# Optimization experiments

Measured on AMD Instinct MI355X. Metric: run time of the kernel, lower is better.

Reference implementation:

```python
import jax, jax.numpy as jnp
import numpy as np

N = 50000          # total nodes (2 types x 25000)
E = 400000         # edges
NEG = 0.2          # leaky_relu negative slope


def _seg_softmax(e, dst, n):
    # softmax over edges grouped by destination node
    m = jax.ops.segment_max(e, dst, num_segments=n)
    m = jnp.where(jnp.isfinite(m), m, 0.0)
    ex = jnp.exp(e - m[dst])
    s = jax.ops.segment_sum(ex, dst, num_segments=n)
    return ex / (s[dst] + 1e-16)


def _gat_conv(h, src, dst, W, al, ar, b, heads, out, res=None, act=None):
    n = h.shape[0]
    ft = (h @ W).reshape(n, heads, out)               # [N,H,D]
    el = jnp.sum(ft * al, axis=-1)                    # [N,H]
    er = jnp.sum(ft * ar, axis=-1)                    # [N,H]
    e = jax.nn.leaky_relu(el[src] + er[dst], NEG)     # [E,H]
    alpha = _seg_softmax(e, dst, n)                   # [E,H]
    rst = jax.ops.segment_sum(ft[src] * alpha[:, :, None], dst, num_segments=n)
    if isinstance(res, str):                          # identity residual (in == heads*out)
        rst = rst + h.reshape(n, heads, out)
    elif res is not None:                             # linear residual projection
        rst = rst + (h @ res).reshape(n, heads, out)
    rst = rst + b                                     # bias [H,D]
    if act is not None:
        rst = act(rst)
    return rst


def setup_inputs() -> dict:
    key = jax.random.key(0)
    ks = jax.random.split(key, 24)
    g = lambda i, shp, s=0.05: jax.random.normal(ks[i], shp, jnp.float32) * s
    inp = {
        "x0": jax.random.normal(ks[0], (25000, 256), jnp.float32),
        "x1": jax.random.normal(ks[1], (25000, 256), jnp.float32),
        "src": jax.random.randint(ks[2], (E,), 0, N, jnp.int32).astype(jnp.int64),
        "dst": jax.random.randint(ks[3], (E,), 0, N, jnp.int32).astype(jnp.int64),
        # per-type input projections
        "fc0_W": g(4, (256, 64)), "fc0_b": jnp.zeros((64,), jnp.float32),
        "fc1_W": g(5, (256, 64)), "fc1_b": jnp.zeros((64,), jnp.float32),
        # layer 0: 64 -> 8 heads x 64
        "W0": g(6, (64, 512)), "al0": g(7, (8, 64)), "ar0": g(8, (8, 64)), "b0": jnp.zeros((8, 64), jnp.float32),
        # layer 1: 512 -> 8 heads x 64 (identity residual)
        "W1": g(9, (512, 512)), "al1": g(10, (8, 64)), "ar1": g(11, (8, 64)), "b1": jnp.zeros((8, 64), jnp.float32),
        # output layer: 512 -> 1 head x 16 (linear residual)
        "W2": g(12, (512, 16)), "al2": g(13, (1, 16)), "ar2": g(14, (1, 16)), "b2": jnp.zeros((1, 16), jnp.float32),
        "resW2": g(15, (512, 16)),
    }
    return inp


def reference(x0, x1, src, dst, fc0_W, fc0_b, fc1_W, fc1_b,
              W0, al0, ar0, b0, W1, al1, ar1, b1,
              W2, al2, ar2, b2, resW2):
    # per-type linear projections, then concat over node axis
    h = jnp.concatenate([x0 @ fc0_W + fc0_b, x1 @ fc1_W + fc1_b], axis=0)  # [N,64]
    h = _gat_conv(h, src, dst, W0, al0, ar0, b0, 8, 64, None, jax.nn.elu).reshape(N, -1)
    h = _gat_conv(h, src, dst, W1, al1, ar1, b1, 8, 64, "id", jax.nn.elu).reshape(N, -1)
    encoded = h
    logits = _gat_conv(h, src, dst, W2, al2, ar2, b2, 1, 16, resW2, None).mean(axis=1)  # [N,16]
    return (logits, encoded)
```

## Files before the change

kernel.cpp:

```cpp
#include <hip/hip_runtime.h>
#include <hip/hip_bf16.h>
#include <math.h>

typedef __hip_bfloat16 bf16;
typedef __attribute__((ext_vector_type(8))) short short8;
typedef __attribute__((ext_vector_type(8))) unsigned short ushort8;
typedef __attribute__((ext_vector_type(4))) float floatx4;

#define NNODES 50000
#define NHALF  25000
#define NEDGES 400000
#define NEG_SLOPE 0.2f

__device__ __forceinline__ float b2f(bf16 x){ return __bfloat162float(x); }
__device__ __forceinline__ bf16  f2b(float x){ return __float2bfloat16(x); }
__device__ __forceinline__ float u2f(unsigned short u){ return __uint_as_float(((unsigned)u) << 16); }

__device__ __forceinline__ float loadF(const void* p, long i, int f32){
  return f32 ? ((const float*)p)[i] : b2f(((const bf16*)p)[i]);
}
__device__ __forceinline__ void storeOut(void* p, long i, float v, int f32){
  if (f32) ((float*)p)[i] = v; else ((bf16*)p)[i] = f2b(v);
}

__device__ __forceinline__ void gl_lds16(const bf16* g, short* l){
  __builtin_amdgcn_global_load_lds(
      (const __attribute__((address_space(1))) unsigned int*)g,
      (__attribute__((address_space(3))) unsigned int*)l, 16, 0, 0);
}

__global__ void k_detect(const unsigned short* __restrict__ x0u,
                         const unsigned* __restrict__ dstu,
                         int* __restrict__ flags)
{
  __shared__ int sh_insane;
  __shared__ unsigned sh_or;
  if (threadIdx.x == 0) { sh_insane = 0; sh_or = 0u; }
  __syncthreads();
  int insane = 0; unsigned orv = 0u;
  for (int i = threadIdx.x; i < 2048; i += 256) {
    unsigned short w = x0u[2 * i];
    int ex = (w >> 7) & 0xFF;
    if (w != 0 && (ex < 108 || ex > 142)) insane++;
    orv |= dstu[2 * i + 1];
  }
  atomicAdd(&sh_insane, insane);
  atomicOr(&sh_or, orv);
  __syncthreads();
  if (threadIdx.x == 0) {
    flags[0] = (sh_insane > 512) ? 1 : 0;
    flags[1] = (sh_or == 0u) ? 1 : 0;
  }
}

__global__ void k_conv_idx(const int* __restrict__ sraw, const int* __restrict__ draw,
                           int* __restrict__ s32, int* __restrict__ d32,
                           int* __restrict__ deg,
                           const int* __restrict__ flags)
{
  int e = blockIdx.x * blockDim.x + threadIdx.x;
  if (e >= NEDGES) return;
  int stride = flags[1] ? 2 : 1;
  int s = sraw[(long)e * stride];
  int d = draw[(long)e * stride];
  s32[e] = s;
  d32[e] = d;
  atomicAdd(&deg[d], 1);
}

struct WSrc { const void* p[17]; int n[17]; };

__global__ void k_canon(WSrc w, bf16* __restrict__ out, const int* __restrict__ flags,
                        int total)
{
  int f32 = flags[0];
  for (int t = blockIdx.x * blockDim.x + threadIdx.x; t < total;
       t += gridDim.x * blockDim.x) {
    int idx = t, k = 0;
    while (idx >= w.n[k]) { idx -= w.n[k]; k++; }
    out[t] = f2b(loadF(w.p[k], idx, f32));
  }
}

__global__ void k_convx(const void* __restrict__ x0, const void* __restrict__ x1,
                        bf16* __restrict__ xb, const int* __restrict__ flags)
{
  long t = (long)blockIdx.x * blockDim.x + threadIdx.x;
  if (t >= (long)NNODES * 256) return;
  int f32 = flags[0];
  long half = (long)NHALF * 256;
  float v = (t < half) ? loadF(x0, t, f32) : loadF(x1, t - half, f32);
  xb[t] = f2b(v);
}

__global__ void k_wt(const bf16* __restrict__ W, bf16* __restrict__ Wt,
                     int K, int M, int Mpad)
{
  int t = blockIdx.x * blockDim.x + threadIdx.x;
  if (t >= Mpad * K) return;
  int m = t / K, k = t % K;
  Wt[t] = (m < M) ? W[(long)k * M + m] : f2b(0.f);
}

__global__ __launch_bounds__(256) void k_gemm_mfma(
    const bf16* __restrict__ A, const bf16* __restrict__ Wt,
    bf16* __restrict__ C, int N, int K, int ldc, int Mout,
    const bf16* __restrict__ bias)
{
  __shared__ __align__(16) short lsA[128 * 32];
  __shared__ __align__(16) short lsB[128 * 32];
  int tid = threadIdx.x;
  int wave = tid >> 6, lane = tid & 63;
  int wm = wave >> 1, wn = wave & 1;
  int rowBase = blockIdx.x * 128;
  int colBase = blockIdx.y * 128;

  floatx4 acc[4][4] = {};
  int laneRow = lane >> 2;
  int laneCol = (lane & 3) * 8;
  int cA0 = wave * 2, cA1 = cA0 + 1;

  for (int kb = 0; kb < K; kb += 32) {
    int r0 = rowBase + cA0 * 16 + laneRow; if (r0 > N - 1) r0 = N - 1;
    int r1 = rowBase + cA1 * 16 + laneRow; if (r1 > N - 1) r1 = N - 1;
    gl_lds16(A + (size_t)r0 * K + kb + laneCol, &lsA[cA0 * 512]);
    gl_lds16(A + (size_t)r1 * K + kb + laneCol, &lsA[cA1 * 512]);
    int m0 = colBase + cA0 * 16 + laneRow;
    int m1 = colBase + cA1 * 16 + laneRow;
    gl_lds16(Wt + (size_t)m0 * K + kb + laneCol, &lsB[cA0 * 512]);
    gl_lds16(Wt + (size_t)m1 * K + kb + laneCol, &lsB[cA1 * 512]);
    __syncthreads();

    short8 af[4], bfr[4];
    int lr = lane & 15, q8 = (lane >> 4) * 8;
    #pragma unroll
    for (int mt = 0; mt < 4; ++mt)
      af[mt] = *(const short8*)&lsA[(wm * 64 + mt * 16 + lr) * 32 + q8];
    #pragma unroll
    for (int nt = 0; nt < 4; ++nt)
      bfr[nt] = *(const short8*)&lsB[(wn * 64 + nt * 16 + lr) * 32 + q8];
    #pragma unroll
    for (int mt = 0; mt < 4; ++mt)
      #pragma unroll
      for (int nt = 0; nt < 4; ++nt)
        acc[mt][nt] = __builtin_amdgcn_mfma_f32_16x16x32_bf16(
            af[mt], bfr[nt], acc[mt][nt], 0, 0, 0);
    __syncthreads();
  }

  int lc = lane & 15, rq = (lane >> 4) * 4;
  #pragma unroll
  for (int mt = 0; mt < 4; ++mt) {
    #pragma unroll
    for (int nt = 0; nt < 4; ++nt) {
      int col = colBase + wn * 64 + nt * 16 + lc;
      if (col >= Mout) continue;
      float bsv = bias ? b2f(bias[col]) : 0.f;
      #pragma unroll
      for (int r = 0; r < 4; ++r) {
        int row = rowBase + wm * 64 + mt * 16 + rq + r;
        if (row < N) C[(size_t)row * ldc + col] = f2b(acc[mt][nt][r] + bsv);
      }
    }
  }
}

__global__ __launch_bounds__(256) void k_elr8(
    const bf16* __restrict__ ft,
    const bf16* __restrict__ al, const bf16* __restrict__ ar,
    float* __restrict__ el, float* __restrict__ er,
    float* __restrict__ part)
{
  __shared__ float sal[512], sar[512];
  __shared__ float redA[32], redB[32];
  for (int i = threadIdx.x; i < 512; i += 256) { sal[i] = b2f(al[i]); sar[i] = b2f(ar[i]); }
  __syncthreads();
  int tid = threadIdx.x;
  int t = blockIdx.x * 256 + tid;
  float a = -1e30f, b = -1e30f;
  if (t < NNODES * 8) {
    int n = t >> 3, h = t & 7;
    const unsigned short* f = (const unsigned short*)ft + (size_t)n * 512 + h * 64;
    float aa = 0.f, bb = 0.f;
    #pragma unroll
    for (int j = 0; j < 8; ++j) {
      ushort8 v = *(const ushort8*)&f[j * 8];
      #pragma unroll
      for (int k = 0; k < 8; ++k) {
        float x = u2f(v[k]);
        aa += x * sal[h * 64 + j * 8 + k];
        bb += x * sar[h * 64 + j * 8 + k];
      }
    }
    a = aa; b = bb;
    el[t] = a; er[t] = b;
  }
  #pragma unroll
  for (int off = 8; off <= 32; off <<= 1) {
    a = fmaxf(a, __shfl_xor(a, off));
    b = fmaxf(b, __shfl_xor(b, off));
  }
  int wave = tid >> 6, lane = tid & 63;
  if (lane < 8) { redA[wave * 8 + lane] = a; redB[wave * 8 + lane] = b; }
  __syncthreads();
  if (tid < 8) {
    float ma = -1e30f, mb = -1e30f;
    #pragma unroll
    for (int w2 = 0; w2 < 4; ++w2) {
      ma = fmaxf(ma, redA[w2 * 8 + tid]);
      mb = fmaxf(mb, redB[w2 * 8 + tid]);
    }
    part[blockIdx.x * 16 + tid]     = ma;
    part[blockIdx.x * 16 + 8 + tid] = mb;
  }
}

__global__ __launch_bounds__(256) void k_elr1(
    const bf16* __restrict__ ft2,
    const bf16* __restrict__ al, const bf16* __restrict__ ar,
    float* __restrict__ el, float* __restrict__ er,
    float* __restrict__ part)
{
  __shared__ float rA[4], rB[4];
  int tid = threadIdx.x;
  int n = blockIdx.x * 256 + tid;
  float a = -1e30f, b = -1e30f;
  if (n < NNODES) {
    const unsigned short* f = (const unsigned short*)ft2 + (size_t)n * 32;
    float aa = 0.f, bb = 0.f;
    #pragma unroll
    for (int d = 0; d < 16; ++d) {
      float x = u2f(f[d]);
      aa += x * b2f(al[d]);
      bb += x * b2f(ar[d]);
    }
    a = aa; b = bb;
    el[n] = a; er[n] = b;
  }
  #pragma unroll
  for (int off = 1; off <= 32; off <<= 1) {
    a = fmaxf(a, __shfl_xor(a, off));
    b = fmaxf(b, __shfl_xor(b, off));
  }
  int wave = tid >> 6, lane = tid & 63;
  if (lane == 0) { rA[wave] = a; rB[wave] = b; }
  __syncthreads();
  if (tid == 0) {
    float ma = -1e30f, mb = -1e30f;
    #pragma unroll
    for (int w2 = 0; w2 < 4; ++w2) { ma = fmaxf(ma, rA[w2]); mb = fmaxf(mb, rB[w2]); }
    part[blockIdx.x * 2]     = ma;
    part[blockIdx.x * 2 + 1] = mb;
  }
}

__global__ void k_maxfin(const float* __restrict__ part, float* __restrict__ M,
                         int nblk, int H)
{
  __shared__ float sm[256];
  __shared__ float sm2[16];
  int tid = threadIdx.x;
  int TH = 2 * H;
  int s = tid % TH, c = tid / TH;
  int nch = 256 / TH;
  float m = -1e30f;
  for (int b = c; b < nblk; b += nch) m = fmaxf(m, part[b * TH + s]);
  sm[tid] = m;
  __syncthreads();
  if (tid < TH) {
    float mm = -1e30f;
    for (int c2 = 0; c2 < nch; ++c2) mm = fmaxf(mm, sm[c2 * TH + tid]);
    sm2[tid] = mm;
  }
  __syncthreads();
  if (tid < H) {
    float v = sm2[tid] + sm2[H + tid];
    M[tid] = v > 0.f ? v : NEG_SLOPE * v;
  }
}

__global__ __launch_bounds__(1024) void k_bsum(const int* __restrict__ deg,
                                               int* __restrict__ bsum, int n)
{
  __shared__ int ws[16];
  int tid = threadIdx.x, lane = tid & 63, wv = tid >> 6;
  int i = blockIdx.x * 1024 + tid;
  int v = (i < n) ? deg[i] : 0;
  #pragma unroll
  for (int off = 1; off < 64; off <<= 1) v += __shfl_xor(v, off);
  if (lane == 0) ws[wv] = v;
  __syncthreads();
  if (tid < 16) {
    int s = ws[tid];
    #pragma unroll
    for (int off = 1; off < 16; off <<= 1) s += __shfl_xor(s, off);
    if (tid == 0) bsum[blockIdx.x] = s;
  }
}

__global__ void k_bscan(int* __restrict__ bsum, int* __restrict__ row_start,
                        int nb, int n)
{
  int lane = threadIdx.x;
  int v = (lane < nb) ? bsum[lane] : 0;
  int x = v;
  #pragma unroll
  for (int off = 1; off < 64; off <<= 1) {
    int y = __shfl_up(x, off);
    if (lane >= off) x += y;
  }
  if (lane < nb) bsum[lane] = x - v;
  if (lane == 63) row_start[n] = x;
}

__global__ __launch_bounds__(1024) void k_scan2(const int* __restrict__ deg,
                                                const int* __restrict__ boff,
                                                int* __restrict__ row_start, int n)
{
  __shared__ int ws[16];
  int tid = threadIdx.x, lane = tid & 63, wv = tid >> 6;
  int i = blockIdx.x * 1024 + tid;
  int v = (i < n) ? deg[i] : 0;
  int x = v;
  #pragma unroll
  for (int off = 1; off < 64; off <<= 1) {
    int y = __shfl_up(x, off);
    if (lane >= off) x += y;
  }
  if (lane == 63) ws[wv] = x;
  __syncthreads();
  if (wv == 0 && lane < 16) {
    int s = ws[lane];
    int xs = s;
    #pragma unroll
    for (int off = 1; off < 16; off <<= 1) {
      int y = __shfl_up(xs, off);
      if (lane >= off) xs += y;
    }
    ws[lane] = xs - s;
  }
  __syncthreads();
  if (i < n) row_start[i] = boff[blockIdx.x] + ws[wv] + x - v;
}

__global__ void k_fill(const int* __restrict__ src, const int* __restrict__ dst,
                       int* __restrict__ cursor, int* __restrict__ csr_src, int E)
{
  int e = blockIdx.x * blockDim.x + threadIdx.x;
  if (e < E) {
    int p = atomicAdd(&cursor[dst[e]], 1);
    csr_src[p] = src[e];
  }
}

__global__ __launch_bounds__(256) void k_agg8(
    const int* __restrict__ row_start, const int* __restrict__ csr_src,
    const float* __restrict__ el, const float* __restrict__ er,
    const float* __restrict__ M,
    const bf16* __restrict__ ft, const bf16* __restrict__ hin,
    const bf16* __restrict__ bias,
    bf16* __restrict__ hout, void* __restrict__ dout, long dout_off,
    const int* __restrict__ flags, int mode)
{
  int wv = (int)((blockIdx.x * blockDim.x + threadIdx.x) >> 6);
  int lane = threadIdx.x & 63;
  if (wv >= NNODES) return;
  int n = wv, g = lane >> 3;
  int st = row_start[n], en = row_start[n + 1];
  float Mh  = M[g];
  float ern = er[n * 8 + g];

  const unsigned short* ftS = (const unsigned short*)ft;
  float ssum = 0.f;
  float acc[8] = {};
  int i = st;
  for (; i + 4 <= en; i += 4) {
    int sn0 = csr_src[i],     sn1 = csr_src[i + 1];
    int sn2 = csr_src[i + 2], sn3 = csr_src[i + 3];
    float e0 = el[sn0 * 8 + g], e1 = el[sn1 * 8 + g];
    float e2 = el[sn2 * 8 + g], e3 = el[sn3 * 8 + g];
    ushort8 r0 = *(const ushort8*)&ftS[(size_t)sn0 * 512 + lane * 8];
    ushort8 r1 = *(const ushort8*)&ftS[(size_t)sn1 * 512 + lane * 8];
    ushort8 r2 = *(const ushort8*)&ftS[(size_t)sn2 * 512 + lane * 8];
    ushort8 r3 = *(const ushort8*)&ftS[(size_t)sn3 * 512 + lane * 8];
    float v0 = e0 + ern, v1 = e1 + ern, v2 = e2 + ern, v3 = e3 + ern;
    v0 = v0 > 0.f ? v0 : NEG_SLOPE * v0;
    v1 = v1 > 0.f ? v1 : NEG_SLOPE * v1;
    v2 = v2 > 0.f ? v2 : NEG_SLOPE * v2;
    v3 = v3 > 0.f ? v3 : NEG_SLOPE * v3;
    float w0 = __expf(v0 - Mh), w1 = __expf(v1 - Mh);
    float w2 = __expf(v2 - Mh), w3 = __expf(v3 - Mh);
    ssum += (w0 + w1) + (w2 + w3);
    #pragma unroll
    for (int j = 0; j < 8; ++j)
      acc[j] += (w0 * u2f(r0[j]) + w1 * u2f(r1[j]))
              + (w2 * u2f(r2[j]) + w3 * u2f(r3[j]));
  }
  for (; i < en; ++i) {
    int sn = csr_src[i];
    float v0 = el[sn * 8 + g] + ern;
    v0 = v0 > 0.f ? v0 : NEG_SLOPE * v0;
    float w0 = __expf(v0 - Mh);
    ushort8 r0 = *(const ushort8*)&ftS[(size_t)sn * 512 + lane * 8];
    ssum += w0;
    #pragma unroll
    for (int j = 0; j < 8; ++j)
      acc[j] += w0 * u2f(r0[j]);
  }

  float inv = ssum > 0.f ? 1.f / ssum : 0.f;
  int f32 = flags[0];
  short8 outv;
  float rr[8];
  #pragma unroll
  for (int j = 0; j < 8; ++j) {
    int col = lane * 8 + j;
    float r = acc[j] * inv + b2f(bias[col]);
    if (mode == 1) r += b2f(hin[(size_t)n * 512 + col]);
    r = r > 0.f ? r : expm1f(r);
    rr[j] = r;
    bf16 o = f2b(r);
    outv[j] = *(short*)&o;
  }
  *(short8*)&hout[(size_t)n * 512 + lane * 8] = outv;
  if (dout) {
    if (f32) {
      floatx4 o0, o1;
      #pragma unroll
      for (int j = 0; j < 4; ++j) { o0[j] = rr[j]; o1[j] = rr[j + 4]; }
      float* dp = (float*)dout + dout_off + (size_t)n * 512 + lane * 8;
      *(floatx4*)dp = o0;
      *(floatx4*)(dp + 4) = o1;
    } else {
      *(short8*)&((bf16*)dout)[dout_off + (size_t)n * 512 + lane * 8] = outv;
    }
  }
}

__global__ __launch_bounds__(256) void k_agg1(
    const int* __restrict__ row_start, const int* __restrict__ csr_src,
    const float* __restrict__ el, const float* __restrict__ er,
    const float* __restrict__ M,
    const bf16* __restrict__ ft2, const bf16* __restrict__ bias,
    void* __restrict__ dout, const int* __restrict__ flags)
{
  int wv = (int)((blockIdx.x * blockDim.x + threadIdx.x) >> 6);
  int lane = threadIdx.x & 63;
  if (wv >= NNODES) return;
  int n = wv, sub = lane >> 4, d = lane & 15;
  int st = row_start[n], en = row_start[n + 1];
  float M0 = M[0];
  float ern = er[n];
  float ssum = 0.f, acc = 0.f;
  for (int i = st + sub; i < en; i += 4) {
    int sn = csr_src[i];
    float v = el[sn] + ern;
    v = v > 0.f ? v : NEG_SLOPE * v;
    float ex = __expf(v - M0);
    acc  += ex * b2f(ft2[(size_t)sn * 32 + d]);
    ssum += ex;
  }
  acc  += __shfl_xor(acc, 16);  acc  += __shfl_xor(acc, 32);
  ssum += __shfl_xor(ssum, 16); ssum += __shfl_xor(ssum, 32);
  if (sub == 0) {
    float inv = ssum > 0.f ? 1.f / ssum : 0.f;
    float r = acc * inv + b2f(bias[d]) + b2f(ft2[(size_t)n * 32 + 16 + d]);
    storeOut(dout, (size_t)n * 16 + d, r, flags[0]);
  }
}

extern "C" void kernel_launch(void* const* d_in, const int* in_sizes, int n_in,
                              void* d_out, int out_size, void* d_ws, size_t ws_size,
                              hipStream_t stream)
{
  const void* x0   = d_in[0];
  const void* x1   = d_in[1];
  const int*  srcR = (const int*)d_in[2];
  const int*  dstR = (const int*)d_in[3];

  char* p = (char*)d_ws;
  auto alloc = [&](size_t bytes) { char* r = p; p += (bytes + 255) & ~(size_t)255; return r; };
  int*      flags     = (int*)  alloc(256);
  bf16*     wc        = (bf16*) alloc((size_t)347312 * 2);
  int*      src32     = (int*)  alloc((size_t)NEDGES * 4);
  int*      dst32     = (int*)  alloc((size_t)NEDGES * 4);
  bf16*     xb        = (bf16*) alloc((size_t)NNODES * 256 * 2);
  bf16*     h0        = (bf16*) alloc((size_t)NNODES * 64 * 2);
  bf16*     hB        = (bf16*) alloc((size_t)NNODES * 512 * 2);
  bf16*     ft        = (bf16*) alloc((size_t)NNODES * 512 * 2);
  bf16*     ft2       = (bf16*) alloc((size_t)NNODES * 32 * 2);
  float*    el        = (float*)alloc((size_t)NNODES * 8 * 4);
  float*    er        = (float*)alloc((size_t)NNODES * 8 * 4);
  int*      deg       = (int*)  alloc((size_t)NNODES * 4);
  int*      row_start = (int*)  alloc((size_t)(NNODES + 1) * 4);
  int*      cursor    = (int*)  alloc((size_t)NNODES * 4);
  int*      csr_src   = (int*)  alloc((size_t)NEDGES * 4);
  int*      bsum      = (int*)  alloc((size_t)64 * 4);
  float*    maxpart   = (float*)alloc((size_t)1600 * 16 * 4);
  float*    Mbuf      = (float*)alloc(256);
  bf16*     fc0t      = (bf16*) alloc((size_t)128 * 256 * 2);
  bf16*     fc1t      = (bf16*) alloc((size_t)128 * 256 * 2);
  bf16*     W0t       = (bf16*) alloc((size_t)512 * 64 * 2);
  bf16*     W1t       = (bf16*) alloc((size_t)512 * 512 * 2);
  bf16*     W2c       = (bf16*) alloc((size_t)128 * 512 * 2);

  const int B = 256;
  auto blk = [](long total, int b) { return (unsigned)((total + b - 1) / b); };
  const int NSCB = (NNODES + 1023) / 1024;

  k_detect<<<1, 256, 0, stream>>>((const unsigned short*)x0, (const unsigned*)dstR, flags);
  hipMemsetAsync(deg, 0, (size_t)NNODES * 4, stream);
  k_conv_idx<<<blk(NEDGES, B), B, 0, stream>>>(srcR, dstR, src32, dst32, deg, flags);

  WSrc wsrc;
  const int widx[17] = {4,5,6,7, 8,9,10,11, 12,13,14,15, 16,17,18,19, 20};
  const int wn[17]   = {16384,64,16384,64, 32768,512,512,512, 262144,512,512,512,
                        8192,16,16,16, 8192};
  int wtotal = 0;
  for (int i = 0; i < 17; ++i) { wsrc.p[i] = d_in[widx[i]]; wsrc.n[i] = wn[i]; wtotal += wn[i]; }
  k_canon<<<blk(wtotal, B), B, 0, stream>>>(wsrc, wc, flags, wtotal);
  k_convx<<<blk((long)NNODES * 256, B), B, 0, stream>>>(x0, x1, xb, flags);

  long woff[18]; woff[0] = 0;
  for (int i = 0; i < 17; ++i) woff[i + 1] = woff[i] + wn[i];
  const bf16 *fc0W = wc + woff[0],  *fc0b = wc + woff[1];
  const bf16 *fc1W = wc + woff[2],  *fc1b = wc + woff[3];
  const bf16 *W0   = wc + woff[4],  *al0  = wc + woff[5],  *ar0 = wc + woff[6],  *b0 = wc + woff[7];
  const bf16 *W1   = wc + woff[8],  *al1  = wc + woff[9],  *ar1 = wc + woff[10], *b1 = wc + woff[11];
  const bf16 *W2   = wc + woff[12], *al2  = wc + woff[13], *ar2 = wc + woff[14], *b2 = wc + woff[15];
  const bf16 *resW2= wc + woff[16];

  k_wt<<<blk(128 * 256, B), B, 0, stream>>>(fc0W, fc0t, 256, 64, 128);
  k_wt<<<blk(128 * 256, B), B, 0, stream>>>(fc1W, fc1t, 256, 64, 128);
  k_wt<<<blk(512 * 64, B), B, 0, stream>>>(W0, W0t, 64, 512, 512);
  k_wt<<<blk(512 * 512, B), B, 0, stream>>>(W1, W1t, 512, 512, 512);
  k_wt<<<blk(128 * 512, B), B, 0, stream>>>(W2, W2c, 512, 16, 128);
  k_wt<<<blk(16 * 512, B), B, 0, stream>>>(resW2, W2c + 16 * 512, 512, 16, 16);

  k_bsum <<<NSCB, 1024, 0, stream>>>(deg, bsum, NNODES);
  k_bscan<<<1, 64, 0, stream>>>(bsum, row_start, NSCB, NNODES);
  k_scan2<<<NSCB, 1024, 0, stream>>>(deg, bsum, row_start, NNODES);
  hipMemcpyAsync(cursor, row_start, (size_t)NNODES * 4, hipMemcpyDeviceToDevice, stream);
  k_fill<<<blk(NEDGES, B), B, 0, stream>>>(src32, dst32, cursor, csr_src, NEDGES);

  auto gemm = [&](const bf16* A, const bf16* Wt, bf16* C, int N, int K,
                  int ldc, int Mout, int ytiles, const bf16* bias) {
    dim3 g(blk(N, 128), ytiles);
    k_gemm_mfma<<<g, 256, 0, stream>>>(A, Wt, C, N, K, ldc, Mout, bias);
  };

  gemm(xb, fc0t, h0, NHALF, 256, 64, 64, 1, fc0b);
  gemm(xb + (size_t)NHALF * 256, fc1t, h0 + (size_t)NHALF * 64, NHALF, 256, 64, 64, 1, fc1b);

  unsigned aggGrid = blk((long)NNODES * 64, B);
  unsigned nblk8 = blk((long)NNODES * 8, B);
  unsigned nblk1 = blk(NNODES, B);

  gemm(h0, W0t, ft, NNODES, 64, 512, 512, 4, nullptr);
  k_elr8<<<nblk8, B, 0, stream>>>(ft, al0, ar0, el, er, maxpart);
  k_maxfin<<<1, 256, 0, stream>>>(maxpart, Mbuf, (int)nblk8, 8);
  k_agg8<<<aggGrid, B, 0, stream>>>(row_start, csr_src, el, er, Mbuf, ft, nullptr, b0,
                                    hB, nullptr, 0, flags, 0);

  gemm(hB, W1t, ft, NNODES, 512, 512, 512, 4, nullptr);
  k_elr8<<<nblk8, B, 0, stream>>>(ft, al1, ar1, el, er, maxpart);
  k_maxfin<<<1, 256, 0, stream>>>(maxpart, Mbuf, (int)nblk8, 8);
  k_agg8<<<aggGrid, B, 0, stream>>>(row_start, csr_src, el, er, Mbuf, ft, hB, b1,
                                    hB, d_out, (long)NNODES * 16, flags, 1);

  gemm(hB, W2c, ft2, NNODES, 512, 32, 32, 1, nullptr);
  k_elr1<<<nblk1, B, 0, stream>>>(ft2, al2, ar2, el, er, maxpart);
  k_maxfin<<<1, 256, 0, stream>>>(maxpart, Mbuf, (int)nblk1, 1);
  k_agg1<<<aggGrid, B, 0, stream>>>(row_start, csr_src, el, er, Mbuf, ft2, b2, d_out, flags);
}
```

Measured before the change: 764.8 us.

## Cut kernel launches: atomic global max, fused weight transposes, vectorized input convert

The separate max-finalize kernels are replaced by order-preserving float encoding plus atomicMax from each block, with the leaky-relu of the combined max done in the aggregation kernels. The six weight-transpose launches are folded into the canonicalization kernel, which writes transposed layouts directly after a memset zeroes the padding. The cursor copy is folded into the scan kernel, and the input conversion now moves 8 elements per thread with vector loads. The aim is fewer launches and less small-kernel overhead, at the cost of atomic contention on a few words and an extra memset.

```diff
diff --git a/kernel.cpp b/kernel.cpp
--- a/kernel.cpp
+++ b/kernel.cpp
@@ -21,6 +21,15 @@
 }
 __device__ __forceinline__ void storeOut(void* p, long i, float v, int f32){
   if (f32) ((float*)p)[i] = v; else ((bf16*)p)[i] = f2b(v);
+}
+
+__device__ __forceinline__ unsigned fenc(float f){
+  unsigned b = __float_as_uint(f);
+  return (b & 0x80000000u) ? ~b : (b | 0x80000000u);
+}
+__device__ __forceinline__ float fdec(unsigned k){
+  unsigned b = (k & 0x80000000u) ? (k & 0x7fffffffu) : ~k;
+  return __uint_as_float(b);
 }
 
 __device__ __forceinline__ void gl_lds16(const bf16* g, short* l){
@@ -68,38 +77,47 @@
   atomicAdd(&deg[d], 1);
 }
 
-struct WSrc { const void* p[17]; int n[17]; };
-
-__global__ void k_canon(WSrc w, bf16* __restrict__ out, const int* __restrict__ flags,
-                        int total)
+struct WSrc { const void* p[17]; void* dst[17]; int n[17]; int M[17]; int st[17]; };
+
+__global__ void k_canon(WSrc w, const int* __restrict__ flags, int total)
 {
   int f32 = flags[0];
   for (int t = blockIdx.x * blockDim.x + threadIdx.x; t < total;
        t += gridDim.x * blockDim.x) {
     int idx = t, k = 0;
     while (idx >= w.n[k]) { idx -= w.n[k]; k++; }
-    out[t] = f2b(loadF(w.p[k], idx, f32));
+    bf16 v = f2b(loadF(w.p[k], idx, f32));
+    if (w.M[k] == 0) {
+      ((bf16*)w.dst[k])[idx] = v;
+    } else {
+      int m = idx % w.M[k], kk = idx / w.M[k];
+      ((bf16*)w.dst[k])[(long)m * w.st[k] + kk] = v;
+    }
   }
 }
 
 __global__ void k_convx(const void* __restrict__ x0, const void* __restrict__ x1,
                         bf16* __restrict__ xb, const int* __restrict__ flags)
 {
-  long t = (long)blockIdx.x * blockDim.x + threadIdx.x;
+  long t = (long)(blockIdx.x * blockDim.x + threadIdx.x) * 8;
   if (t >= (long)NNODES * 256) return;
-  int f32 = flags[0];
   long half = (long)NHALF * 256;
-  float v = (t < half) ? loadF(x0, t, f32) : loadF(x1, t - half, f32);
-  xb[t] = f2b(v);
-}
-
-__global__ void k_wt(const bf16* __restrict__ W, bf16* __restrict__ Wt,
-                     int K, int M, int Mpad)
-{
-  int t = blockIdx.x * blockDim.x + threadIdx.x;
-  if (t >= Mpad * K) return;
-  int m = t / K, k = t % K;
-  Wt[t] = (m < M) ? W[(long)k * M + m] : f2b(0.f);
+  const void* src = (t < half) ? x0 : x1;
+  long off = (t < half) ? t : t - half;
+  short8 o;
+  if (flags[0]) {
+    const float* f = (const float*)src + off;
+    floatx4 a = *(const floatx4*)f;
+    floatx4 b = *(const floatx4*)(f + 4);
+    #pragma unroll
+    for (int j = 0; j < 4; ++j) {
+      bf16 x = f2b(a[j]); o[j] = *(short*)&x;
+      bf16 y = f2b(b[j]); o[j + 4] = *(short*)&y;
+    }
+  } else {
+    o = *(const short8*)((const bf16*)src + off);
+  }
+  *(short8*)(xb + t) = o;
 }
 
 __global__ __launch_bounds__(256) void k_gemm_mfma(
@@ -169,7 +187,7 @@
     const bf16* __restrict__ ft,
     const bf16* __restrict__ al, const bf16* __restrict__ ar,
     float* __restrict__ el, float* __restrict__ er,
-    float* __restrict__ part)
+    unsigned* __restrict__ Menc)
 {
   __shared__ float sal[512], sar[512];
   __shared__ float redA[32], redB[32];
@@ -210,8 +228,8 @@
       ma = fmaxf(ma, redA[w2 * 8 + tid]);
       mb = fmaxf(mb, redB[w2 * 8 + tid]);
     }
-    part[blockIdx.x * 16 + tid]     = ma;
-    part[blockIdx.x * 16 + 8 + tid] = mb;
+    atomicMax(&Menc[tid], fenc(ma));
+    atomicMax(&Menc[8 + tid], fenc(mb));
   }
 }
 
@@ -219,7 +237,7 @@
     const bf16* __restrict__ ft2,
     const bf16* __restrict__ al, const bf16* __restrict__ ar,
     float* __restrict__ el, float* __restrict__ er,
-    float* __restrict__ part)
+    unsigned* __restrict__ Menc)
 {
   __shared__ float rA[4], rB[4];
   int tid = threadIdx.x;
@@ -249,33 +267,8 @@
     float ma = -1e30f, mb = -1e30f;
     #pragma unroll
     for (int w2 = 0; w2 < 4; ++w2) { ma = fmaxf(ma, rA[w2]); mb = fmaxf(mb, rB[w2]); }
-    part[blockIdx.x * 2]     = ma;
-    part[blockIdx.x * 2 + 1] = mb;
-  }
-}
-
-__global__ void k_maxfin(const float* __restrict__ part, float* __restrict__ M,
-                         int nblk, int H)
-{
-  __shared__ float sm[256];
-  __shared__ float sm2[16];
-  int tid = threadIdx.x;
-  int TH = 2 * H;
-  int s = tid % TH, c = tid / TH;
-  int nch = 256 / TH;
-  float m = -1e30f;
-  for (int b = c; b < nblk; b += nch) m = fmaxf(m, part[b * TH + s]);
-  sm[tid] = m;
-  __syncthreads();
-  if (tid < TH) {
-    float mm = -1e30f;
-    for (int c2 = 0; c2 < nch; ++c2) mm = fmaxf(mm, sm[c2 * TH + tid]);
-    sm2[tid] = mm;
-  }
-  __syncthreads();
-  if (tid < H) {
-    float v = sm2[tid] + sm2[H + tid];
-    M[tid] = v > 0.f ? v : NEG_SLOPE * v;
+    atomicMax(&Menc[0], fenc(ma));
+    atomicMax(&Menc[1], fenc(mb));
   }
 }
 
@@ -315,7 +308,8 @@
 
 __global__ __launch_bounds__(1024) void k_scan2(const int* __restrict__ deg,
                                                 const int* __restrict__ boff,
-                                                int* __restrict__ row_start, int n)
+                                                int* __restrict__ row_start,
+                                                int* __restrict__ cursor, int n)
 {
   __shared__ int ws[16];
   int tid = threadIdx.x, lane = tid & 63, wv = tid >> 6;
@@ -340,7 +334,11 @@
     ws[lane] = xs - s;
   }
   __syncthreads();
-  if (i < n) row_start[i] = boff[blockIdx.x] + ws[wv] + x - v;
+  if (i < n) {
+    int val = boff[blockIdx.x] + ws[wv] + x - v;
+    row_start[i] = val;
+    cursor[i] = val;
+  }
 }
 
 __global__ void k_fill(const int* __restrict__ src, const int* __restrict__ dst,
@@ -356,7 +354,7 @@
 __global__ __launch_bounds__(256) void k_agg8(
     const int* __restrict__ row_start, const int* __restrict__ csr_src,
     const float* __restrict__ el, const float* __restrict__ er,
-    const float* __restrict__ M,
+    const unsigned* __restrict__ Menc,
     const bf16* __restrict__ ft, const bf16* __restrict__ hin,
     const bf16* __restrict__ bias,
     bf16* __restrict__ hout, void* __restrict__ dout, long dout_off,
@@ -367,7 +365,8 @@
   if (wv >= NNODES) return;
   int n = wv, g = lane >> 3;
   int st = row_start[n], en = row_start[n + 1];
-  float Mh  = M[g];
+  float mm = fdec(Menc[g]) + fdec(Menc[8 + g]);
+  float Mh = mm > 0.f ? mm : NEG_SLOPE * mm;
   float ern = er[n * 8 + g];
 
   const unsigned short* ftS = (const unsigned short*)ft;
@@ -440,7 +439,7 @@
 __global__ __launch_bounds__(256) void k_agg1(
     const int* __restrict__ row_start, const int* __restrict__ csr_src,
     const float* __restrict__ el, const float* __restrict__ er,
-    const float* __restrict__ M,
+    const unsigned* __restrict__ Menc,
     const bf16* __restrict__ ft2, const bf16* __restrict__ bias,
     void* __restrict__ dout, const int* __restrict__ flags)
 {
@@ -449,7 +448,8 @@
   if (wv >= NNODES) return;
   int n = wv, sub = lane >> 4, d = lane & 15;
   int st = row_start[n], en = row_start[n + 1];
-  float M0 = M[0];
+  float mm = fdec(Menc[0]) + fdec(Menc[1]);
+  float M0 = mm > 0.f ? mm : NEG_SLOPE * mm;
   float ern = er[n];
   float ssum = 0.f, acc = 0.f;
   for (int i = st + sub; i < en; i += 4) {
@@ -496,51 +496,55 @@
   int*      cursor    = (int*)  alloc((size_t)NNODES * 4);
   int*      csr_src   = (int*)  alloc((size_t)NEDGES * 4);
   int*      bsum      = (int*)  alloc((size_t)64 * 4);
-  float*    maxpart   = (float*)alloc((size_t)1600 * 16 * 4);
-  float*    Mbuf      = (float*)alloc(256);
+  unsigned* Menc      = (unsigned*)alloc(256);
   bf16*     fc0t      = (bf16*) alloc((size_t)128 * 256 * 2);
   bf16*     fc1t      = (bf16*) alloc((size_t)128 * 256 * 2);
   bf16*     W0t       = (bf16*) alloc((size_t)512 * 64 * 2);
   bf16*     W1t       = (bf16*) alloc((size_t)512 * 512 * 2);
   bf16*     W2c       = (bf16*) alloc((size_t)128 * 512 * 2);
+  size_t twBytes = ((size_t)128*256 + 128*256 + 512*64 + 512*512 + 128*512) * 2;
 
   const int B = 256;
   auto blk = [](long total, int b) { return (unsigned)((total + b - 1) / b); };
   const int NSCB = (NNODES + 1023) / 1024;
 
+  hipMemsetAsync(deg, 0, (size_t)NNODES * 4, stream);
+  hipMemsetAsync(Menc, 0, 256, stream);
+  hipMemsetAsync(fc0t, 0, twBytes, stream);
+
   k_detect<<<1, 256, 0, stream>>>((const unsigned short*)x0, (const unsigned*)dstR, flags);
-  hipMemsetAsync(deg, 0, (size_t)NNODES * 4, stream);
   k_conv_idx<<<blk(NEDGES, B), B, 0, stream>>>(srcR, dstR, src32, dst32, deg, flags);
 
-  WSrc wsrc;
+  long woff[18]; woff[0] = 0;
   const int widx[17] = {4,5,6,7, 8,9,10,11, 12,13,14,15, 16,17,18,19, 20};
   const int wn[17]   = {16384,64,16384,64, 32768,512,512,512, 262144,512,512,512,
                         8192,16,16,16, 8192};
+  for (int i = 0; i < 17; ++i) woff[i + 1] = woff[i] + wn[i];
+
+  WSrc wsrc;
   int wtotal = 0;
-  for (int i = 0; i < 17; ++i) { wsrc.p[i] = d_in[widx[i]]; wsrc.n[i] = wn[i]; wtotal += wn[i]; }
-  k_canon<<<blk(wtotal, B), B, 0, stream>>>(wsrc, wc, flags, wtotal);
-  k_convx<<<blk((long)NNODES * 256, B), B, 0, stream>>>(x0, x1, xb, flags);
-
-  long woff[18]; woff[0] = 0;
-  for (int i = 0; i < 17; ++i) woff[i + 1] = woff[i] + wn[i];
-  const bf16 *fc0W = wc + woff[0],  *fc0b = wc + woff[1];
-  const bf16 *fc1W = wc + woff[2],  *fc1b = wc + woff[3];
-  const bf16 *W0   = wc + woff[4],  *al0  = wc + woff[5],  *ar0 = wc + woff[6],  *b0 = wc + woff[7];
-  const bf16 *W1   = wc + woff[8],  *al1  = wc + woff[9],  *ar1 = wc + woff[10], *b1 = wc + woff[11];
-  const bf16 *W2   = wc + woff[12], *al2  = wc + woff[13], *ar2 = wc + woff[14], *b2 = wc + woff[15];
-  const bf16 *resW2= wc + woff[16];
-
-  k_wt<<<blk(128 * 256, B), B, 0, stream>>>(fc0W, fc0t, 256, 64, 128);
-  k_wt<<<blk(128 * 256, B), B, 0, stream>>>(fc1W, fc1t, 256, 64, 128);
-  k_wt<<<blk(512 * 64, B), B, 0, stream>>>(W0, W0t, 64, 512, 512);
-  k_wt<<<blk(512 * 512, B), B, 0, stream>>>(W1, W1t, 512, 512, 512);
-  k_wt<<<blk(128 * 512, B), B, 0, stream>>>(W2, W2c, 512, 16, 128);
-  k_wt<<<blk(16 * 512, B), B, 0, stream>>>(resW2, W2c + 16 * 512, 512, 16, 16);
+  for (int i = 0; i < 17; ++i) {
+    wsrc.p[i] = d_in[widx[i]]; wsrc.n[i] = wn[i];
+    wsrc.dst[i] = wc + woff[i]; wsrc.M[i] = 0; wsrc.st[i] = 0;
+    wtotal += wn[i];
+  }
+  wsrc.dst[0]  = fc0t;            wsrc.M[0]  = 64;  wsrc.st[0]  = 256;
+  wsrc.dst[2]  = fc1t;            wsrc.M[2]  = 64;  wsrc.st[2]  = 256;
+  wsrc.dst[4]  = W0t;             wsrc.M[4]  = 512; wsrc.st[4]  = 64;
+  wsrc.dst[8]  = W1t;             wsrc.M[8]  = 512; wsrc.st[8]  = 512;
+  wsrc.dst[12] = W2c;             wsrc.M[12] = 16;  wsrc.st[12] = 512;
+  wsrc.dst[16] = W2c + 16 * 512;  wsrc.M[16] = 16;  wsrc.st[16] = 512;
+  k_canon<<<blk(wtotal, B), B, 0, stream>>>(wsrc, flags, wtotal);
+  k_convx<<<blk((long)NNODES * 32, B), B, 0, stream>>>(x0, x1, xb, flags);
+
+  const bf16 *fc0b = wc + woff[1], *fc1b = wc + woff[3];
+  const bf16 *al0  = wc + woff[5],  *ar0 = wc + woff[6],  *b0 = wc + woff[7];
+  const bf16 *al1  = wc + woff[9],  *ar1 = wc + woff[10], *b1 = wc + woff[11];
+  const bf16 *al2  = wc + woff[13], *ar2 = wc + woff[14], *b2 = wc + woff[15];
 
   k_bsum <<<NSCB, 1024, 0, stream>>>(deg, bsum, NNODES);
   k_bscan<<<1, 64, 0, stream>>>(bsum, row_start, NSCB, NNODES);
-  k_scan2<<<NSCB, 1024, 0, stream>>>(deg, bsum, row_start, NNODES);
-  hipMemcpyAsync(cursor, row_start, (size_t)NNODES * 4, hipMemcpyDeviceToDevice, stream);
+  k_scan2<<<NSCB, 1024, 0, stream>>>(deg, bsum, row_start, cursor, NNODES);
   k_fill<<<blk(NEDGES, B), B, 0, stream>>>(src32, dst32, cursor, csr_src, NEDGES);
 
   auto gemm = [&](const bf16* A, const bf16* Wt, bf16* C, int N, int K,
@@ -557,19 +561,16 @@
   unsigned nblk1 = blk(NNODES, B);
 
   gemm(h0, W0t, ft, NNODES, 64, 512, 512, 4, nullptr);
-  k_elr8<<<nblk8, B, 0, stream>>>(ft, al0, ar0, el, er, maxpart);
-  k_maxfin<<<1, 256, 0, stream>>>(maxpart, Mbuf, (int)nblk8, 8);
-  k_agg8<<<aggGrid, B, 0, stream>>>(row_start, csr_src, el, er, Mbuf, ft, nullptr, b0,
+  k_elr8<<<nblk8, B, 0, stream>>>(ft, al0, ar0, el, er, Menc);
+  k_agg8<<<aggGrid, B, 0, stream>>>(row_start, csr_src, el, er, Menc, ft, nullptr, b0,
                                     hB, nullptr, 0, flags, 0);
 
   gemm(hB, W1t, ft, NNODES, 512, 512, 512, 4, nullptr);
-  k_elr8<<<nblk8, B, 0, stream>>>(ft, al1, ar1, el, er, maxpart);
-  k_maxfin<<<1, 256, 0, stream>>>(maxpart, Mbuf, (int)nblk8, 8);
-  k_agg8<<<aggGrid, B, 0, stream>>>(row_start, csr_src, el, er, Mbuf, ft, hB, b1,
+  k_elr8<<<nblk8, B, 0, stream>>>(ft, al1, ar1, el, er, Menc + 16);
+  k_agg8<<<aggGrid, B, 0, stream>>>(row_start, csr_src, el, er, Menc + 16, ft, hB, b1,
                                     hB, d_out, (long)NNODES * 16, flags, 1);
 
   gemm(hB, W2c, ft2, NNODES, 512, 32, 32, 1, nullptr);
-  k_elr1<<<nblk1, B, 0, stream>>>(ft2, al2, ar2, el, er, maxpart);
-  k_maxfin<<<1, 256, 0, stream>>>(maxpart, Mbuf, (int)nblk1, 1);
-  k_agg1<<<aggGrid, B, 0, stream>>>(row_start, csr_src, el, er, Mbuf, ft2, b2, d_out, flags);
-}
+  k_elr1<<<nblk1, B, 0, stream>>>(ft2, al2, ar2, el, er, Menc + 32);
+  k_agg1<<<aggGrid, B, 0, stream>>>(row_start, csr_src, el, er, Menc + 32, ft2, b2, d_out, flags);
+}
```

Result: faster. 749.1 us (-2.1%).
